# Optimization experiments

Measured on AMD Instinct MI355X. Metric: run time of the kernel, lower is better.

Reference implementation:

```python
import jax, jax.numpy as jnp
import numpy as np

N_NODES = 100000
N_EDGES = 1600000
NODE_DIM = 128
EDGE_DIM = 64
HID = 64
N_POSTS = 10000


def _gru_cell(x, h, w_ih, w_hh, b_ih, b_hh):
    # torch.nn.GRUCell semantics
    gi = x @ w_ih.T + b_ih          # [N, 3H]
    gh = h @ w_hh.T + b_hh          # [N, 3H]
    i_r, i_z, i_n = jnp.split(gi, 3, axis=-1)
    h_r, h_z, h_n = jnp.split(gh, 3, axis=-1)
    r = jax.nn.sigmoid(i_r + h_r)
    z = jax.nn.sigmoid(i_z + h_z)
    n = jnp.tanh(i_n + r * h_n)
    return (1.0 - z) * n + z * h


def setup_inputs() -> dict:
    key = jax.random.key(0)
    ks = jax.random.split(key, 20)
    s = 0.05
    f32 = jnp.float32
    return {
        "node_features": jax.random.normal(ks[0], (N_NODES, NODE_DIM), dtype=f32),
        "edge_attr": jax.random.normal(ks[1], (N_EDGES, EDGE_DIM), dtype=f32),
        "edge_index": jax.random.randint(ks[2], (2, N_EDGES), 0, N_NODES),
        "post_mask": jax.random.randint(ks[3], (N_POSTS,), 0, N_NODES),
        "n_layers": 2,
        # node_encoder
        "W_node": jax.random.normal(ks[4], (HID, NODE_DIM), dtype=f32) * s,
        "b_node": jnp.zeros((HID,), dtype=f32),
        # edge_encoder
        "W_edge": jax.random.normal(ks[5], (HID, EDGE_DIM), dtype=f32) * s,
        "b_edge": jnp.zeros((HID,), dtype=f32),
        # message_aggregator: Linear(2H -> H)
        "W_agg": jax.random.normal(ks[6], (HID, 2 * HID), dtype=f32) * s,
        "b_agg": jnp.zeros((HID,), dtype=f32),
        # GRUCell(H, H)
        "w_ih": jax.random.normal(ks[7], (3 * HID, HID), dtype=f32) * s,
        "w_hh": jax.random.normal(ks[8], (3 * HID, HID), dtype=f32) * s,
        "b_ih": jnp.zeros((3 * HID,), dtype=f32),
        "b_hh": jnp.zeros((3 * HID,), dtype=f32),
        # output MLP: H -> H//2 -> 1
        "W_out1": jax.random.normal(ks[9], (HID // 2, HID), dtype=f32) * s,
        "b_out1": jnp.zeros((HID // 2,), dtype=f32),
        "W_out2": jax.random.normal(ks[10], (1, HID // 2), dtype=f32) * s,
        "b_out2": jnp.zeros((1,), dtype=f32),
    }


def reference(node_features, edge_attr, edge_index, post_mask, n_layers,
              W_node, b_node, W_edge, b_edge, W_agg, b_agg,
              w_ih, w_hh, b_ih, b_hh, W_out1, b_out1, W_out2, b_out2):
    h = jax.nn.relu(node_features @ W_node.T + b_node)       # [N, H]
    e = jax.nn.relu(edge_attr @ W_edge.T + b_edge)           # [E, H]
    src, dst = edge_index[0], edge_index[1]
    for _ in range(int(n_layers)):
        # batched gather-concat-linear (replaces per-edge python loop)
        msg = jnp.concatenate([h[src], e], axis=1) @ W_agg.T + b_agg  # [E, H]
        messages = jax.ops.segment_sum(msg, dst, num_segments=N_NODES)  # scatter-add
        h = _gru_cell(messages, h, w_ih, w_hh, b_ih, b_hh)
    p = h[post_mask]                                          # [P, H]
    logits = (jax.nn.relu(p @ W_out1.T + b_out1) @ W_out2.T + b_out2).squeeze(-1)
    return jax.nn.sigmoid(logits)
```

## Files before the change

### kernel.cpp

```cpp
#include <hip/hip_runtime.h>

using short8  = __attribute__((ext_vector_type(8))) short;
using ushort8 = __attribute__((ext_vector_type(8))) unsigned short;
using us4     = __attribute__((ext_vector_type(4))) unsigned short;
using f32x4   = __attribute__((ext_vector_type(4))) float;

static __device__ __forceinline__ short f2bf(float f) {
  unsigned u = __float_as_uint(f);
  u += 0x7fffu + ((u >> 16) & 1u);
  return (short)(u >> 16);
}
static __device__ __forceinline__ float bf2f(short s) {
  return __uint_as_float(((unsigned)(unsigned short)s) << 16);
}
static __device__ __forceinline__ float us2f(unsigned short s) {
  return __uint_as_float(((unsigned)s) << 16);
}
static __device__ __forceinline__ short8 load8_bf16(const float* __restrict__ p) {
  const f32x4* q = (const f32x4*)p;
  f32x4 a = q[0], b = q[1];
  short8 r;
  r[0]=f2bf(a[0]); r[1]=f2bf(a[1]); r[2]=f2bf(a[2]); r[3]=f2bf(a[3]);
  r[4]=f2bf(b[0]); r[5]=f2bf(b[1]); r[6]=f2bf(b[2]); r[7]=f2bf(b[3]);
  return r;
}
static __device__ __forceinline__ void split8(const float* p, short8& hi, short8& lo) {
  const f32x4* q = (const f32x4*)p;
  f32x4 a = q[0], b = q[1];
  float v[8] = {a[0],a[1],a[2],a[3],b[0],b[1],b[2],b[3]};
#pragma unroll
  for (int j = 0; j < 8; ++j) {
    short h = f2bf(v[j]);
    hi[j] = h;
    lo[j] = f2bf(v[j] - bf2f(h));
  }
}

__global__ __launch_bounds__(256) void node_encode(
    const float* __restrict__ X, const float* __restrict__ Wn,
    const float* __restrict__ bn, float* __restrict__ h,
    unsigned short* __restrict__ hb, int nNodes) {
  int tid = threadIdx.x, lane = tid & 63, w = tid >> 6, lg = lane >> 4, lr = lane & 15;
  short8 bf[4][4];
#pragma unroll
  for (int t = 0; t < 4; ++t)
#pragma unroll
    for (int kk = 0; kk < 4; ++kk)
      bf[t][kk] = load8_bf16(Wn + (t*16+lr)*128 + kk*32 + lg*8);
  float bias[4];
#pragma unroll
  for (int t = 0; t < 4; ++t) bias[t] = bn[t*16+lr];

  int base = blockIdx.x * 64 + w * 16;
  int arow = base + lr;
  int nn = arow < nNodes ? arow : nNodes - 1;
  f32x4 acc[4] = {};
#pragma unroll
  for (int kk = 0; kk < 4; ++kk) {
    short8 aH, aL;
    split8(X + (size_t)nn*128 + kk*32 + lg*8, aH, aL);
#pragma unroll
    for (int t = 0; t < 4; ++t) {
      acc[t] = __builtin_amdgcn_mfma_f32_16x16x32_bf16(aH, bf[t][kk], acc[t], 0, 0, 0);
      acc[t] = __builtin_amdgcn_mfma_f32_16x16x32_bf16(aL, bf[t][kk], acc[t], 0, 0, 0);
    }
  }
#pragma unroll
  for (int t = 0; t < 4; ++t)
#pragma unroll
    for (int i = 0; i < 4; ++i) {
      int orow = base + lg*4 + i;
      if (orow < nNodes) {
        float v = fmaxf(acc[t][i] + bias[t], 0.f);
        h[(size_t)orow*64 + t*16 + lr] = v;
        hb[(size_t)orow*64 + t*16 + lr] = (unsigned short)f2bf(v);
      }
    }
}

__global__ __launch_bounds__(256) void hist_deg(
    const int* __restrict__ dst, int* __restrict__ deg, int nEdges) {
  for (int e = blockIdx.x*256 + threadIdx.x; e < nEdges; e += gridDim.x*256)
    atomicAdd(&deg[dst[e]], 1);
}

__global__ __launch_bounds__(256) void scan_pass1(
    const int* __restrict__ deg, int* __restrict__ bsum, int n) {
  int b = blockIdx.x, tid = threadIdx.x;
  int base = b * 4096;
  int s = 0;
  for (int j = tid; j < 4096; j += 256) {
    int i = base + j;
    s += (i < n) ? deg[i] : 0;
  }
  __shared__ int ws[4];
#pragma unroll
  for (int o = 32; o; o >>= 1) s += __shfl_down(s, o);
  if ((tid & 63) == 0) ws[tid >> 6] = s;
  __syncthreads();
  if (tid == 0) bsum[b] = ws[0] + ws[1] + ws[2] + ws[3];
}

__global__ void scan_pass2(const int* __restrict__ bsum, int* __restrict__ boff,
                           int* __restrict__ off, int nBlocks, int n) {
  if (threadIdx.x == 0 && blockIdx.x == 0) {
    int run = 0;
    for (int b = 0; b < nBlocks; ++b) { boff[b] = run; run += bsum[b]; }
    off[n] = run;
  }
}

__global__ __launch_bounds__(256) void scan_pass3(
    const int* __restrict__ deg, const int* __restrict__ boff,
    int* __restrict__ off, int n) {
  int b = blockIdx.x, tid = threadIdx.x;
  int lane = tid & 63, w = tid >> 6;
  int base = b * 4096 + tid * 16;
  int d[16], tot = 0;
#pragma unroll
  for (int j = 0; j < 16; ++j) {
    d[j] = (base + j < n) ? deg[base + j] : 0;
    tot += d[j];
  }
  int s = tot;
#pragma unroll
  for (int o = 1; o < 64; o <<= 1) {
    int t = __shfl_up(s, o);
    if (lane >= o) s += t;
  }
  __shared__ int ws[4];
  if (lane == 63) ws[w] = s;
  __syncthreads();
  int wo = 0;
  for (int k = 0; k < 4; ++k) wo += (k < w) ? ws[k] : 0;
  int run = boff[b] + wo + s - tot;
#pragma unroll
  for (int j = 0; j < 16; ++j) {
    if (base + j < n) off[base + j] = run;
    run += d[j];
  }
}

__global__ __launch_bounds__(256) void edge_mlp(
    const float* __restrict__ EA, const float* __restrict__ We,
    const float* __restrict__ be, const int* __restrict__ src,
    const int* __restrict__ dst, const int* __restrict__ off,
    int* __restrict__ cur, int* __restrict__ srcs,
    unsigned short* __restrict__ encb, int nEdges) {
  int tid = threadIdx.x, lane = tid & 63, w = tid >> 6;
  int lr = lane & 15, lg = lane >> 4;

  short8 bf[4][2];
#pragma unroll
  for (int t = 0; t < 4; ++t)
#pragma unroll
    for (int kk = 0; kk < 2; ++kk)
      bf[t][kk] = load8_bf16(We + (t*16+lr)*64 + kk*32 + lg*8);
  float bias[4];
#pragma unroll
  for (int t = 0; t < 4; ++t) bias[t] = be[t*16+lr];

  int e0 = blockIdx.x * 128 + w * 32;
  int pos_reg = 0;
  if (lane < 32) {
    int e = e0 + lane;
    if (e < nEdges) {
      int d = dst[e];
      pos_reg = off[d] + atomicAdd(&cur[d], 1);
      srcs[pos_reg] = src[e];
    }
  }

  int c0 = e0 + lr;      if (c0 >= nEdges) c0 = nEdges - 1;
  int c1 = e0 + 16 + lr; if (c1 >= nEdges) c1 = nEdges - 1;
  const float* p0 = EA + (size_t)c0 * 64;
  const float* p1 = EA + (size_t)c1 * 64;
  f32x4 acc[2][4] = {};
#pragma unroll
  for (int kk = 0; kk < 2; ++kk) {
    short8 a0 = load8_bf16(p0 + kk*32 + lg*8);
    short8 a1 = load8_bf16(p1 + kk*32 + lg*8);
#pragma unroll
    for (int t = 0; t < 4; ++t) {
      acc[0][t] = __builtin_amdgcn_mfma_f32_16x16x32_bf16(a0, bf[t][kk], acc[0][t], 0,0,0);
      acc[1][t] = __builtin_amdgcn_mfma_f32_16x16x32_bf16(a1, bf[t][kk], acc[1][t], 0,0,0);
    }
  }
#pragma unroll
  for (int b = 0; b < 2; ++b)
#pragma unroll
    for (int i = 0; i < 4; ++i) {
      int rloc = b*16 + lg*4 + i;
      int e = e0 + rloc;
      int pos = __shfl(pos_reg, rloc);
      if (e < nEdges) {
        us4 v;
#pragma unroll
        for (int t = 0; t < 4; ++t)
          v[t] = (unsigned short)f2bf(fmaxf(acc[b][t][i] + bias[t], 0.f));
        *(us4*)(encb + (size_t)pos*64 + lr*4) = v;
      }
    }
}

__global__ __launch_bounds__(256) void seg_sum(
    const unsigned short* __restrict__ encb, const int* __restrict__ off,
    float* __restrict__ Esum, int nNodes) {
  int tid = threadIdx.x, lane = tid & 63, w = tid >> 6;
  int er = lane >> 3, fs = lane & 7;
  int n0 = (blockIdx.x * 4 + w) * 4;
  if (n0 >= nNodes) return;
  int a[4], b[4];
#pragma unroll
  for (int j = 0; j < 4; ++j) {
    int n = n0 + j;
    a[j] = (n < nNodes) ? off[n] : 0;
    b[j] = (n < nNodes) ? off[n + 1] : 0;
  }
  float acc[4][8];
#pragma unroll
  for (int j = 0; j < 4; ++j)
#pragma unroll
    for (int q = 0; q < 8; ++q) acc[j][q] = 0.f;
  int mx = 0;
#pragma unroll
  for (int j = 0; j < 4; ++j) { int c = b[j] - a[j]; if (c > mx) mx = c; }
  for (int t = 0; t < mx; t += 8) {
#pragma unroll
    for (int j = 0; j < 4; ++j) {
      int i0 = a[j] + t + er;
      if (i0 < b[j]) {
        ushort8 v = *(const ushort8*)(encb + (size_t)i0*64 + fs*8);
#pragma unroll
        for (int q = 0; q < 8; ++q) acc[j][q] += us2f(v[q]);
      }
    }
  }
#pragma unroll
  for (int j = 0; j < 4; ++j)
#pragma unroll
    for (int q = 0; q < 8; ++q) {
      float v = acc[j][q];
      v += __shfl_xor(v, 8);
      v += __shfl_xor(v, 16);
      v += __shfl_xor(v, 32);
      acc[j][q] = v;
    }
  if (er == 0) {
#pragma unroll
    for (int j = 0; j < 4; ++j) {
      int n = n0 + j;
      if (n < nNodes) {
        f32x4 lo = {acc[j][0], acc[j][1], acc[j][2], acc[j][3]};
        f32x4 hi = {acc[j][4], acc[j][5], acc[j][6], acc[j][7]};
        *(f32x4*)(Esum + (size_t)n * 64 + fs * 8) = lo;
        *(f32x4*)(Esum + (size_t)n * 64 + fs * 8 + 4) = hi;
      }
    }
  }
}

__global__ __launch_bounds__(256) void make_combos(
    const float* __restrict__ wih, const float* __restrict__ Wagg,
    const float* __restrict__ bagg, const float* __restrict__ whh,
    short* __restrict__ WceH, short* __restrict__ WceL,
    short* __restrict__ WchH, short* __restrict__ WchL,
    short* __restrict__ whhH, short* __restrict__ whhL, float* __restrict__ bihA) {
  int idx = blockIdx.x*256 + threadIdx.x;
  if (idx < 12288) {
    int r = idx >> 6, k = idx & 63;
    float a = 0.f, b = 0.f;
    for (int j = 0; j < 64; ++j) {
      float ww = wih[r*64 + j];
      a += ww * Wagg[j*128 + k];
      b += ww * Wagg[j*128 + 64 + k];
    }
    short ah = f2bf(a);
    WchH[idx] = ah; WchL[idx] = f2bf(a - bf2f(ah));
    int kp = (k & 15) * 4 + (k >> 4);
    short bh = f2bf(b);
    WceH[r*64 + kp] = bh; WceL[r*64 + kp] = f2bf(b - bf2f(bh));
    float wv = whh[idx];
    short hh = f2bf(wv);
    whhH[idx] = hh; whhL[idx] = f2bf(wv - bf2f(hh));
    if (idx < 192) {
      float s = 0.f;
      for (int j = 0; j < 64; ++j) s += wih[idx*64 + j] * bagg[j];
      bihA[idx] = s;
    }
  }
}

__global__ __launch_bounds__(256) void gather_G(
    const unsigned short* __restrict__ hb, const int* __restrict__ off,
    const int* __restrict__ srcs, float* __restrict__ G, int nNodes) {
  int tid = threadIdx.x, lane = tid & 63, w = tid >> 6;
  int er = lane >> 3, fs = lane & 7;
  int n0 = (blockIdx.x * 4 + w) * 4;
  if (n0 >= nNodes) return;
  int a[4], b[4];
#pragma unroll
  for (int j = 0; j < 4; ++j) {
    int n = n0 + j;
    a[j] = (n < nNodes) ? off[n] : 0;
    b[j] = (n < nNodes) ? off[n + 1] : 0;
  }
  float acc[4][8];
#pragma unroll
  for (int j = 0; j < 4; ++j)
#pragma unroll
    for (int q = 0; q < 8; ++q) acc[j][q] = 0.f;
  int mx = 0;
#pragma unroll
  for (int j = 0; j < 4; ++j) { int c = b[j] - a[j]; if (c > mx) mx = c; }
  for (int t = 0; t < mx; t += 16) {
    int s0[4], s1[4];
    bool m0[4], m1[4];
#pragma unroll
    for (int j = 0; j < 4; ++j) {
      int i0 = a[j] + t + er, i1 = i0 + 8;
      int bm = b[j] - 1;
      m0[j] = i0 < b[j]; m1[j] = i1 < b[j];
      int c0 = m0[j] ? i0 : (bm > a[j] ? bm : a[j]);
      int c1 = m1[j] ? i1 : c0;
      s0[j] = (b[j] > a[j]) ? srcs[c0] : 0;
      s1[j] = (b[j] > a[j]) ? srcs[c1] : 0;
    }
#pragma unroll
    for (int j = 0; j < 4; ++j) {
      ushort8 v0 = *(const ushort8*)(hb + (size_t)s0[j] * 64 + fs * 8);
      ushort8 v1 = *(const ushort8*)(hb + (size_t)s1[j] * 64 + fs * 8);
      if (m0[j]) {
#pragma unroll
        for (int q = 0; q < 8; ++q) acc[j][q] += us2f(v0[q]);
      }
      if (m1[j]) {
#pragma unroll
        for (int q = 0; q < 8; ++q) acc[j][q] += us2f(v1[q]);
      }
    }
  }
#pragma unroll
  for (int j = 0; j < 4; ++j)
#pragma unroll
    for (int q = 0; q < 8; ++q) {
      float v = acc[j][q];
      v += __shfl_xor(v, 8);
      v += __shfl_xor(v, 16);
      v += __shfl_xor(v, 32);
      acc[j][q] = v;
    }
  if (er == 0) {
#pragma unroll
    for (int j = 0; j < 4; ++j) {
      int n = n0 + j;
      if (n < nNodes) {
        f32x4 lo = {acc[j][0], acc[j][1], acc[j][2], acc[j][3]};
        f32x4 hi = {acc[j][4], acc[j][5], acc[j][6], acc[j][7]};
        *(f32x4*)(G + (size_t)n * 64 + fs * 8) = lo;
        *(f32x4*)(G + (size_t)n * 64 + fs * 8 + 4) = hi;
      }
    }
  }
}

__global__ __launch_bounds__(256) void layer_dense(
    const float* __restrict__ h_old, const float* __restrict__ Esum,
    const float* __restrict__ G, const int* __restrict__ deg,
    const short* __restrict__ WceH, const short* __restrict__ WceL,
    const short* __restrict__ WchH, const short* __restrict__ WchL,
    const short* __restrict__ whhH, const short* __restrict__ whhL,
    const float* __restrict__ bihA, const float* __restrict__ bih,
    const float* __restrict__ bhh, float* __restrict__ h_new,
    unsigned short* __restrict__ h_newb, int nNodes) {
  int tid = threadIdx.x, lane = tid & 63, w = tid >> 6;
  int lr = lane & 15, lg = lane >> 4;
  int nb = blockIdx.x * 64;

  int arow = nb + w*16 + lr; if (arow >= nNodes) arow = nNodes - 1;
  short8 EsH[2], EsL[2], GHf[2], GLf[2], HH[2], HL[2];
#pragma unroll
  for (int kk = 0; kk < 2; ++kk) {
    split8(Esum + (size_t)arow*64 + kk*32 + lg*8, EsH[kk], EsL[kk]);
    split8(G + (size_t)arow*64 + kk*32 + lg*8, GHf[kk], GLf[kk]);
    split8(h_old + (size_t)arow*64 + kk*32 + lg*8, HH[kk], HL[kk]);
  }

  int row0 = nb + w*16 + lg*4;
  float degv[4];
#pragma unroll
  for (int i = 0; i < 4; ++i) {
    int n = row0 + i;
    degv[i] = (n < nNodes) ? (float)deg[n] : 0.f;
  }

  f32x4 gi[12], gh[12];
#pragma unroll
  for (int ct = 0; ct < 12; ++ct) {
    float bi = bih[ct*16 + lr], ba = bihA[ct*16 + lr], bh = bhh[ct*16 + lr];
#pragma unroll
    for (int i = 0; i < 4; ++i) { gi[ct][i] = bi + degv[i]*ba; gh[ct][i] = bh; }
  }

#pragma unroll
  for (int ct = 0; ct < 12; ++ct) {
    int wb = (ct*16 + lr)*64 + lg*8;
#pragma unroll
    for (int kk = 0; kk < 2; ++kk) {
      int o = wb + kk*32;
      short8 wceh = *(const short8*)(WceH + o);
      short8 wcel = *(const short8*)(WceL + o);
      short8 wchh = *(const short8*)(WchH + o);
      short8 wchl = *(const short8*)(WchL + o);
      short8 whh_h = *(const short8*)(whhH + o);
      short8 whh_l = *(const short8*)(whhL + o);
      gi[ct] = __builtin_amdgcn_mfma_f32_16x16x32_bf16(EsH[kk], wceh, gi[ct], 0,0,0);
      gi[ct] = __builtin_amdgcn_mfma_f32_16x16x32_bf16(EsL[kk], wceh, gi[ct], 0,0,0);
      gi[ct] = __builtin_amdgcn_mfma_f32_16x16x32_bf16(EsH[kk], wcel, gi[ct], 0,0,0);
      gi[ct] = __builtin_amdgcn_mfma_f32_16x16x32_bf16(GHf[kk], wchh, gi[ct], 0,0,0);
      gi[ct] = __builtin_amdgcn_mfma_f32_16x16x32_bf16(GLf[kk], wchh, gi[ct], 0,0,0);
      gi[ct] = __builtin_amdgcn_mfma_f32_16x16x32_bf16(GHf[kk], wchl, gi[ct], 0,0,0);
      gh[ct] = __builtin_amdgcn_mfma_f32_16x16x32_bf16(HH[kk], whh_h, gh[ct], 0,0,0);
      gh[ct] = __builtin_amdgcn_mfma_f32_16x16x32_bf16(HL[kk], whh_h, gh[ct], 0,0,0);
      gh[ct] = __builtin_amdgcn_mfma_f32_16x16x32_bf16(HH[kk], whh_l, gh[ct], 0,0,0);
    }
  }

#pragma unroll
  for (int ct = 0; ct < 4; ++ct)
#pragma unroll
    for (int i = 0; i < 4; ++i) {
      int n = row0 + i;
      if (n < nNodes) {
        int jh = ct*16 + lr;
        float r = 1.f/(1.f + expf(-(gi[ct][i] + gh[ct][i])));
        float z = 1.f/(1.f + expf(-(gi[ct+4][i] + gh[ct+4][i])));
        float nn = tanhf(gi[ct+8][i] + r * gh[ct+8][i]);
        float hv = h_old[(size_t)n*64 + jh];
        float hn = (1.f - z)*nn + z*hv;
        h_new[(size_t)n*64 + jh] = hn;
        h_newb[(size_t)n*64 + jh] = (unsigned short)f2bf(hn);
      }
    }
}

__global__ __launch_bounds__(256) void out_mlp(
    const float* __restrict__ h, const int* __restrict__ pm,
    const float* __restrict__ W1, const float* __restrict__ b1,
    const float* __restrict__ W2, const float* __restrict__ b2,
    float* __restrict__ out, int nPosts) {
  int tid = threadIdx.x;
  int lane = tid & 63;
  int p = blockIdx.x*4 + (tid >> 6);
  if (p >= nPosts) return;
  int n = pm[p];
  float v = h[(size_t)n*64 + lane];
  int row = lane & 31;
  float o = b1[row];
#pragma unroll
  for (int k = 0; k < 64; ++k) {
    float vb = __shfl(v, k);
    o += vb * W1[row*64 + k];
  }
  o = fmaxf(o, 0.f);
  float val = o * W2[row] * 0.5f;
#pragma unroll
  for (int offm = 32; offm > 0; offm >>= 1) val += __shfl_xor(val, offm);
  if (lane == 0) out[p] = 1.f/(1.f + expf(-(val + b2[0])));
}

static inline char* aln(char*& w, size_t bytes) {
  uintptr_t p = ((uintptr_t)w + 255) & ~(uintptr_t)255;
  char* r = (char*)p;
  w = r + bytes;
  return r;
}

extern "C" void kernel_launch(void* const* d_in, const int* in_sizes, int n_in,
                              void* d_out, int out_size, void* d_ws, size_t ws_size,
                              hipStream_t stream) {
  const float* X    = (const float*)d_in[0];
  const float* EA   = (const float*)d_in[1];
  const int*   EI   = (const int*)d_in[2];
  const int*   PM   = (const int*)d_in[3];
  const float* Wn   = (const float*)d_in[5];
  const float* bn   = (const float*)d_in[6];
  const float* We   = (const float*)d_in[7];
  const float* be   = (const float*)d_in[8];
  const float* Wagg = (const float*)d_in[9];
  const float* bagg = (const float*)d_in[10];
  const float* wih  = (const float*)d_in[11];
  const float* whh  = (const float*)d_in[12];
  const float* bih  = (const float*)d_in[13];
  const float* bhh  = (const float*)d_in[14];
  const float* W1   = (const float*)d_in[15];
  const float* b1   = (const float*)d_in[16];
  const float* W2   = (const float*)d_in[17];
  const float* b2   = (const float*)d_in[18];
  float* out = (float*)d_out;

  int nNodes = in_sizes[0] / 128;
  int nEdges = in_sizes[1] / 64;
  int nPosts = in_sizes[3];
  const int* src = EI;
  const int* dst = EI + nEdges;
  int nSB = (nNodes + 4095) / 4096;

  char* w = (char*)d_ws;
  float* h0   = (float*)aln(w, (size_t)nNodes * 64 * 4);
  float* h1   = (float*)aln(w, (size_t)nNodes * 64 * 4);
  unsigned short* h0b = (unsigned short*)aln(w, (size_t)nNodes * 64 * 2);
  unsigned short* h1b = (unsigned short*)aln(w, (size_t)nNodes * 64 * 2);
  float* Esum = (float*)aln(w, (size_t)nNodes * 64 * 4);
  float* G    = (float*)aln(w, (size_t)nNodes * 64 * 4);
  short* WceH = (short*)aln(w, 12288 * 2);
  short* WceL = (short*)aln(w, 12288 * 2);
  short* WchH = (short*)aln(w, 12288 * 2);
  short* WchL = (short*)aln(w, 12288 * 2);
  short* whhH = (short*)aln(w, 12288 * 2);
  short* whhL = (short*)aln(w, 12288 * 2);
  float* bihA = (float*)aln(w, 192 * 4);
  int*   off  = (int*)aln(w, (size_t)(nNodes + 1) * 4);
  int*   deg  = (int*)aln(w, (size_t)nNodes * 4);
  int*   cur  = (int*)aln(w, (size_t)nNodes * 4);
  int*   srcs = (int*)aln(w, (size_t)nEdges * 4);
  int*   bsum = (int*)aln(w, (size_t)nSB * 4);
  int*   boff = (int*)aln(w, (size_t)nSB * 4);
  unsigned short* encb = (unsigned short*)aln(w, (size_t)nEdges * 64 * 2);

  hipMemsetAsync(deg, 0, (size_t)nNodes * 4, stream);
  hipMemsetAsync(cur, 0, (size_t)nNodes * 4, stream);

  hist_deg<<<2048, 256, 0, stream>>>(dst, deg, nEdges);
  scan_pass1<<<nSB, 256, 0, stream>>>(deg, bsum, nNodes);
  scan_pass2<<<1, 1, 0, stream>>>(bsum, boff, off, nSB, nNodes);
  scan_pass3<<<nSB, 256, 0, stream>>>(deg, boff, off, nNodes);

  node_encode<<<(nNodes + 63) / 64, 256, 0, stream>>>(X, Wn, bn, h0, h0b, nNodes);
  edge_mlp<<<(nEdges + 127) / 128, 256, 0, stream>>>(EA, We, be, src, dst, off, cur,
                                                     srcs, encb, nEdges);
  seg_sum<<<(nNodes + 15) / 16, 256, 0, stream>>>(encb, off, Esum, nNodes);
  make_combos<<<48, 256, 0, stream>>>(wih, Wagg, bagg, whh,
                                      WceH, WceL, WchH, WchL, whhH, whhL, bihA);

  gather_G<<<(nNodes + 15) / 16, 256, 0, stream>>>(h0b, off, srcs, G, nNodes);
  layer_dense<<<(nNodes + 63) / 64, 256, 0, stream>>>(
      h0, Esum, G, deg, WceH, WceL, WchH, WchL, whhH, whhL,
      bihA, bih, bhh, h1, h1b, nNodes);
  gather_G<<<(nNodes + 15) / 16, 256, 0, stream>>>(h1b, off, srcs, G, nNodes);
  layer_dense<<<(nNodes + 63) / 64, 256, 0, stream>>>(
      h1, Esum, G, deg, WceH, WceL, WchH, WchL, whhH, whhL,
      bihA, bih, bhh, h0, h0b, nNodes);

  out_mlp<<<(nPosts + 3) / 4, 256, 0, stream>>>(h0, PM, W1, b1, W2, b2, out, nPosts);
}
```

Baseline: 827.3 us.

## Fuse neighbor gather into GRU layer kernel via shared-memory staging

Merges the gather_G kernel into the dense layer kernel. Each block gathers neighbor hidden sums for its 64 nodes into shared memory and then runs the GRU matmuls, which removes the global G buffer round trip and one launch per layer. The cost is fewer in-flight blocks during the latency-bound gather phase, plus extra shared memory and register pressure that may lower occupancy.

After: 938.8 us. +13.5%, slower.

```diff
diff --git a/kernel.cpp b/kernel.cpp
--- a/kernel.cpp
+++ b/kernel.cpp
@@ -291,98 +291,96 @@
   }
 }
 
-__global__ __launch_bounds__(256) void gather_G(
-    const unsigned short* __restrict__ hb, const int* __restrict__ off,
-    const int* __restrict__ srcs, float* __restrict__ G, int nNodes) {
-  int tid = threadIdx.x, lane = tid & 63, w = tid >> 6;
-  int er = lane >> 3, fs = lane & 7;
-  int n0 = (blockIdx.x * 4 + w) * 4;
-  if (n0 >= nNodes) return;
-  int a[4], b[4];
-#pragma unroll
-  for (int j = 0; j < 4; ++j) {
-    int n = n0 + j;
-    a[j] = (n < nNodes) ? off[n] : 0;
-    b[j] = (n < nNodes) ? off[n + 1] : 0;
-  }
-  float acc[4][8];
-#pragma unroll
-  for (int j = 0; j < 4; ++j)
-#pragma unroll
-    for (int q = 0; q < 8; ++q) acc[j][q] = 0.f;
-  int mx = 0;
-#pragma unroll
-  for (int j = 0; j < 4; ++j) { int c = b[j] - a[j]; if (c > mx) mx = c; }
-  for (int t = 0; t < mx; t += 16) {
-    int s0[4], s1[4];
-    bool m0[4], m1[4];
-#pragma unroll
-    for (int j = 0; j < 4; ++j) {
-      int i0 = a[j] + t + er, i1 = i0 + 8;
-      int bm = b[j] - 1;
-      m0[j] = i0 < b[j]; m1[j] = i1 < b[j];
-      int c0 = m0[j] ? i0 : (bm > a[j] ? bm : a[j]);
-      int c1 = m1[j] ? i1 : c0;
-      s0[j] = (b[j] > a[j]) ? srcs[c0] : 0;
-      s1[j] = (b[j] > a[j]) ? srcs[c1] : 0;
-    }
-#pragma unroll
-    for (int j = 0; j < 4; ++j) {
-      ushort8 v0 = *(const ushort8*)(hb + (size_t)s0[j] * 64 + fs * 8);
-      ushort8 v1 = *(const ushort8*)(hb + (size_t)s1[j] * 64 + fs * 8);
-      if (m0[j]) {
-#pragma unroll
-        for (int q = 0; q < 8; ++q) acc[j][q] += us2f(v0[q]);
-      }
-      if (m1[j]) {
-#pragma unroll
-        for (int q = 0; q < 8; ++q) acc[j][q] += us2f(v1[q]);
-      }
-    }
-  }
-#pragma unroll
-  for (int j = 0; j < 4; ++j)
-#pragma unroll
-    for (int q = 0; q < 8; ++q) {
-      float v = acc[j][q];
-      v += __shfl_xor(v, 8);
-      v += __shfl_xor(v, 16);
-      v += __shfl_xor(v, 32);
-      acc[j][q] = v;
-    }
-  if (er == 0) {
-#pragma unroll
-    for (int j = 0; j < 4; ++j) {
-      int n = n0 + j;
-      if (n < nNodes) {
-        f32x4 lo = {acc[j][0], acc[j][1], acc[j][2], acc[j][3]};
-        f32x4 hi = {acc[j][4], acc[j][5], acc[j][6], acc[j][7]};
-        *(f32x4*)(G + (size_t)n * 64 + fs * 8) = lo;
-        *(f32x4*)(G + (size_t)n * 64 + fs * 8 + 4) = hi;
-      }
-    }
-  }
-}
-
-__global__ __launch_bounds__(256) void layer_dense(
-    const float* __restrict__ h_old, const float* __restrict__ Esum,
-    const float* __restrict__ G, const int* __restrict__ deg,
+__global__ __launch_bounds__(256) void layer_fused(
+    const float* __restrict__ h_old, const unsigned short* __restrict__ h_oldb,
+    const float* __restrict__ Esum,
+    const int* __restrict__ off, const int* __restrict__ srcs,
+    const int* __restrict__ deg,
     const short* __restrict__ WceH, const short* __restrict__ WceL,
     const short* __restrict__ WchH, const short* __restrict__ WchL,
     const short* __restrict__ whhH, const short* __restrict__ whhL,
     const float* __restrict__ bihA, const float* __restrict__ bih,
     const float* __restrict__ bhh, float* __restrict__ h_new,
     unsigned short* __restrict__ h_newb, int nNodes) {
+  __shared__ float G[64][68];
   int tid = threadIdx.x, lane = tid & 63, w = tid >> 6;
   int lr = lane & 15, lg = lane >> 4;
+  int er = lane >> 3, fs = lane & 7;
   int nb = blockIdx.x * 64;
+
+  for (int g = 0; g < 4; ++g) {
+    int n0 = nb + w*16 + g*4;
+    int a[4], b[4];
+#pragma unroll
+    for (int j = 0; j < 4; ++j) {
+      int n = n0 + j;
+      a[j] = (n < nNodes) ? off[n] : 0;
+      b[j] = (n < nNodes) ? off[n + 1] : 0;
+    }
+    float acc[4][8];
+#pragma unroll
+    for (int j = 0; j < 4; ++j)
+#pragma unroll
+      for (int q = 0; q < 8; ++q) acc[j][q] = 0.f;
+    int mx = 0;
+#pragma unroll
+    for (int j = 0; j < 4; ++j) { int c = b[j] - a[j]; if (c > mx) mx = c; }
+    for (int t = 0; t < mx; t += 16) {
+      int s0[4], s1[4];
+      bool m0[4], m1[4];
+#pragma unroll
+      for (int j = 0; j < 4; ++j) {
+        int i0 = a[j] + t + er, i1 = i0 + 8;
+        int bm = b[j] - 1;
+        m0[j] = i0 < b[j]; m1[j] = i1 < b[j];
+        int c0 = m0[j] ? i0 : (bm > a[j] ? bm : a[j]);
+        int c1 = m1[j] ? i1 : c0;
+        s0[j] = (b[j] > a[j]) ? srcs[c0] : 0;
+        s1[j] = (b[j] > a[j]) ? srcs[c1] : 0;
+      }
+#pragma unroll
+      for (int j = 0; j < 4; ++j) {
+        ushort8 v0 = *(const ushort8*)(h_oldb + (size_t)s0[j] * 64 + fs * 8);
+        ushort8 v1 = *(const ushort8*)(h_oldb + (size_t)s1[j] * 64 + fs * 8);
+        if (m0[j]) {
+#pragma unroll
+          for (int q = 0; q < 8; ++q) acc[j][q] += us2f(v0[q]);
+        }
+        if (m1[j]) {
+#pragma unroll
+          for (int q = 0; q < 8; ++q) acc[j][q] += us2f(v1[q]);
+        }
+      }
+    }
+#pragma unroll
+    for (int j = 0; j < 4; ++j)
+#pragma unroll
+      for (int q = 0; q < 8; ++q) {
+        float v = acc[j][q];
+        v += __shfl_xor(v, 8);
+        v += __shfl_xor(v, 16);
+        v += __shfl_xor(v, 32);
+        acc[j][q] = v;
+      }
+    if (er == 0) {
+#pragma unroll
+      for (int j = 0; j < 4; ++j) {
+        int rloc = w*16 + g*4 + j;
+        f32x4 lo = {acc[j][0], acc[j][1], acc[j][2], acc[j][3]};
+        f32x4 hi = {acc[j][4], acc[j][5], acc[j][6], acc[j][7]};
+        *(f32x4*)(&G[rloc][fs*8]) = lo;
+        *(f32x4*)(&G[rloc][fs*8 + 4]) = hi;
+      }
+    }
+  }
+  __syncthreads();
 
   int arow = nb + w*16 + lr; if (arow >= nNodes) arow = nNodes - 1;
   short8 EsH[2], EsL[2], GHf[2], GLf[2], HH[2], HL[2];
 #pragma unroll
   for (int kk = 0; kk < 2; ++kk) {
     split8(Esum + (size_t)arow*64 + kk*32 + lg*8, EsH[kk], EsL[kk]);
-    split8(G + (size_t)arow*64 + kk*32 + lg*8, GHf[kk], GLf[kk]);
+    split8(&G[w*16 + lr][kk*32 + lg*8], GHf[kk], GLf[kk]);
     split8(h_old + (size_t)arow*64 + kk*32 + lg*8, HH[kk], HL[kk]);
   }
 
@@ -512,7 +510,6 @@
   unsigned short* h0b = (unsigned short*)aln(w, (size_t)nNodes * 64 * 2);
   unsigned short* h1b = (unsigned short*)aln(w, (size_t)nNodes * 64 * 2);
   float* Esum = (float*)aln(w, (size_t)nNodes * 64 * 4);
-  float* G    = (float*)aln(w, (size_t)nNodes * 64 * 4);
   short* WceH = (short*)aln(w, 12288 * 2);
   short* WceL = (short*)aln(w, 12288 * 2);
   short* WchH = (short*)aln(w, 12288 * 2);
@@ -543,13 +540,11 @@
   make_combos<<<48, 256, 0, stream>>>(wih, Wagg, bagg, whh,
                                       WceH, WceL, WchH, WchL, whhH, whhL, bihA);
 
-  gather_G<<<(nNodes + 15) / 16, 256, 0, stream>>>(h0b, off, srcs, G, nNodes);
-  layer_dense<<<(nNodes + 63) / 64, 256, 0, stream>>>(
-      h0, Esum, G, deg, WceH, WceL, WchH, WchL, whhH, whhL,
+  layer_fused<<<(nNodes + 63) / 64, 256, 0, stream>>>(
+      h0, h0b, Esum, off, srcs, deg, WceH, WceL, WchH, WchL, whhH, whhL,
       bihA, bih, bhh, h1, h1b, nNodes);
-  gather_G<<<(nNodes + 15) / 16, 256, 0, stream>>>(h1b, off, srcs, G, nNodes);
-  layer_dense<<<(nNodes + 63) / 64, 256, 0, stream>>>(
-      h1, Esum, G, deg, WceH, WceL, WchH, WchL, whhH, whhL,
+  layer_fused<<<(nNodes + 63) / 64, 256, 0, stream>>>(
+      h1, h1b, Esum, off, srcs, deg, WceH, WceL, WchH, WchL, whhH, whhL,
       bihA, bih, bhh, h0, h0b, nNodes);
 
   out_mlp<<<(nPosts + 3) / 4, 256, 0, stream>>>(h0, PM, W1, b1, W2, b2, out, nPosts);
```
